# Optimization experiments

Measured on AMD Instinct MI355X. Metric: run time of the kernel, lower is better.

The kernel has to match this reference:

```python
import jax, jax.numpy as jnp
import numpy as np

CUTOFF = 2.0
LOG2 = float(np.log(2.0))

def ssp(x):
    # shifted softplus: softplus(x) - log(2)
    return jax.nn.softplus(x) - LOG2

def setup_inputs() -> dict:
    key = jax.random.key(0)
    ks = jax.random.split(key, 12)
    N, E, H, F, G = 10000, 320000, 256, 256, 50
    x = jax.random.normal(ks[0], (N, H), dtype=jnp.float32)
    edge_index = jax.random.randint(ks[1], (2, E), 0, N, dtype=jnp.int64)
    edge_weight = jax.random.normal(ks[2], (E, 3), dtype=jnp.float32)
    edge_attr = jax.random.normal(ks[3], (E, G), dtype=jnp.float32)
    s = lambda fan_in: 1.0 / np.sqrt(fan_in)
    mlp_w1 = jax.random.uniform(ks[4], (G, F), jnp.float32, -s(G), s(G))
    mlp_b1 = jax.random.uniform(ks[5], (F,), jnp.float32, -s(G), s(G))
    mlp_w2 = jax.random.uniform(ks[6], (F, F), jnp.float32, -s(F), s(F))
    mlp_b2 = jax.random.uniform(ks[7], (F,), jnp.float32, -s(F), s(F))
    lin1_w = jax.random.uniform(ks[8], (H, F), jnp.float32, -s(H), s(H))
    lin2_w = jax.random.uniform(ks[9], (F, H), jnp.float32, -s(F), s(F))
    lin2_b = jax.random.uniform(ks[10], (H,), jnp.float32, -s(F), s(F))
    return {"x": x, "edge_index": edge_index, "edge_weight": edge_weight,
            "edge_attr": edge_attr, "mlp_w1": mlp_w1, "mlp_b1": mlp_b1,
            "mlp_w2": mlp_w2, "mlp_b2": mlp_b2, "lin1_w": lin1_w,
            "lin2_w": lin2_w, "lin2_b": lin2_b}

def reference(x, edge_index, edge_weight, edge_attr,
              mlp_w1, mlp_b1, mlp_w2, mlp_b2, lin1_w, lin2_w, lin2_b):
    N = x.shape[0]
    # cutoff envelope on edge distances
    distances = jnp.linalg.norm(edge_weight, axis=1)                 # [E]
    C = 0.5 * (jnp.cos(distances * jnp.pi / CUTOFF) + 1.0)
    C = C * (distances <= CUTOFF)                                    # [E]
    # edge filter MLP
    W = ssp(edge_attr @ mlp_w1 + mlp_b1) @ mlp_w2 + mlp_b2           # [E, F]
    W = W * C[:, None]
    i, j = edge_index[0], edge_index[1]
    messages = W * (x[j] @ lin1_w)                                   # [E, F]
    agg = jax.ops.segment_sum(messages, i, num_segments=N)           # [N, F]
    h = ssp(agg @ lin2_w + lin2_b)                                   # [N, H]
    return x + h
```

## Files before the change

### kernel.cpp

```cpp
#include <hip/hip_runtime.h>
#include <hip/hip_bf16.h>
#include <stdint.h>

#define HF 256
#define GG 50

typedef __attribute__((ext_vector_type(8))) short bf16x8;
typedef __attribute__((ext_vector_type(4))) short bf16x4;
typedef __attribute__((ext_vector_type(4))) float f32x4;

__device__ __forceinline__ uint32_t f2bf2u(float a, float b){
    __hip_bfloat162 h = __float22bfloat162_rn(make_float2(a, b));
    union { __hip_bfloat162 h; uint32_t u; } v; v.h = h; return v.u;
}
__device__ __forceinline__ float bf2f(short s){
    union { uint32_t u; float f; } v; v.u = ((uint32_t)(uint16_t)s) << 16;
    return v.f;
}
__device__ __forceinline__ float ssp_f(float x){
    float e = __builtin_amdgcn_exp2f(x * 1.44269504088896341f);
    return 0.69314718055994531f * __builtin_amdgcn_logf(1.0f + e)
         - 0.69314718055994531f;
}

__device__ __forceinline__ void pack_natural(const float* __restrict__ B,
                                             short* __restrict__ Bp,
                                             int idx, int KT, int kmax)
{
    int lane = idx & 63;
    int kt   = (idx >> 6) & (KT - 1);
    int ntg  = idx >> (6 + (KT == 2 ? 1 : 3));
    int col  = ntg * 16 + (lane & 15);
    int k0   = kt * 32 + (lane >> 4) * 8;
    uint32_t u[4];
#pragma unroll
    for (int jj = 0; jj < 4; ++jj) {
        int ka = k0 + 2*jj, kb = ka + 1;
        float a = (ka < kmax) ? B[(size_t)ka * HF + col] : 0.f;
        float b = (kb < kmax) ? B[(size_t)kb * HF + col] : 0.f;
        u[jj] = f2bf2u(a, b);
    }
    *(uint4*)&Bp[(size_t)idx * 8] = *(uint4*)u;
}

__global__ __launch_bounds__(256)
void prep_kernel(const float* __restrict__ w1, const float* __restrict__ b1,
                 const float* __restrict__ w2,
                 const float* __restrict__ lin1, const float* __restrict__ lin2,
                 short* __restrict__ w1p, short* __restrict__ w2p,
                 short* __restrict__ lin1p, short* __restrict__ lin2p,
                 const float* __restrict__ x, short* __restrict__ x_bf, int nx8,
                 const int* __restrict__ eidx, int* __restrict__ cnt, int E,
                 float* __restrict__ agg, int nAgg4, int gConv, int gHist)
{
    int b = blockIdx.x, tid = threadIdx.x;
    if (b < 8) {
        int idx  = b * 256 + tid;
        int lane = idx & 63;
        int kt   = (idx >> 6) & 1;
        int ntg  = idx >> 7;
        int col  = ntg * 16 + (lane & 15);
        int k0   = kt * 32 + (lane >> 4) * 8;
        uint32_t u[4];
#pragma unroll
        for (int jj = 0; jj < 4; ++jj) {
            int ka = k0 + 2*jj, kb = ka + 1;
            float va = (ka < GG) ? w1[(size_t)ka * HF + col]
                                 : ((ka == GG) ? b1[col] : 0.f);
            float vb = (kb < GG) ? w1[(size_t)kb * HF + col]
                                 : ((kb == GG) ? b1[col] : 0.f);
            u[jj] = f2bf2u(va, vb);
        }
        *(uint4*)&w1p[(size_t)idx * 8] = *(uint4*)u;
    } else if (b < 40) {
        int idx = (b - 8) * 256 + tid;
        int lane = idx & 63;
        int kt   = (idx >> 6) & 7;
        int ntg  = idx >> 9;
        int col  = ntg * 16 + (lane & 15);
        int s0   = kt * 32 + (lane >> 4) * 8;
        uint32_t u[4];
#pragma unroll
        for (int jj = 0; jj < 4; ++jj) {
            int sa = s0 + 2*jj, sb = sa + 1;
            int fa = (sa >> 6) * 64 + (sa & 3) * 16 + ((sa & 63) >> 2);
            int fb = (sb >> 6) * 64 + (sb & 3) * 16 + ((sb & 63) >> 2);
            u[jj] = f2bf2u(w2[(size_t)fa * HF + col], w2[(size_t)fb * HF + col]);
        }
        *(uint4*)&w2p[(size_t)idx * 8] = *(uint4*)u;
    } else if (b < 72) {
        pack_natural(lin1, lin1p, (b - 40) * 256 + tid, 8, HF);
    } else if (b < 104) {
        pack_natural(lin2, lin2p, (b - 72) * 256 + tid, 8, HF);
    } else if (b < 104 + gConv) {
        int idx = (b - 104) * 256 + tid;
        if (idx < nx8) {
            const float* xp = x + (size_t)idx * 8;
            float4 p0 = *(const float4*)(xp);
            float4 p1 = *(const float4*)(xp + 4);
            uint32_t u[4] = { f2bf2u(p0.x, p0.y), f2bf2u(p0.z, p0.w),
                              f2bf2u(p1.x, p1.y), f2bf2u(p1.z, p1.w) };
            *(uint4*)&x_bf[(size_t)idx * 8] = *(uint4*)u;
        }
    } else if (b < 104 + gConv + gHist) {
        int e = (b - 104 - gConv) * 256 + tid;
        if (e < E) atomicAdd(&cnt[eidx[e]], 1);
    } else {
        int idx = (b - 104 - gConv - gHist) * 256 + tid;
        if (idx < nAgg4) ((float4*)agg)[idx] = make_float4(0.f, 0.f, 0.f, 0.f);
    }
}

__global__ __launch_bounds__(256)
void scan_kernel(const int* __restrict__ cnt, int* __restrict__ row,
                 int* __restrict__ cursor, int N, int E)
{
    __shared__ int part[256];
    const int t = threadIdx.x;
    const int CH = (N + 255) / 256;
    int lo = t * CH;
    int hi = min(lo + CH, N);
    int s = 0;
    for (int n = lo; n < hi; ++n) s += cnt[n];
    part[t] = s;
    __syncthreads();
    for (int off = 1; off < 256; off <<= 1) {
        int v = (t >= off) ? part[t - off] : 0;
        __syncthreads();
        part[t] += v;
        __syncthreads();
    }
    int acc = part[t] - s;
    for (int n = lo; n < hi; ++n) {
        row[n] = acc; cursor[n] = acc;
        acc += cnt[n];
    }
    if (t == 255) row[N] = E;
}

__global__ __launch_bounds__(256)
void mid_kernel(const int* __restrict__ eidx, int* __restrict__ cursor,
                int* __restrict__ perm, int E, int gScatter,
                const short* __restrict__ x_bf, const short* __restrict__ lin1p,
                short* __restrict__ y_p, int N)
{
    const int tid = threadIdx.x;
    if ((int)blockIdx.x < gScatter) {
        int e = blockIdx.x * 256 + tid;
        if (e < E) {
            int pos = atomicAdd(&cursor[eidx[e]], 1);
            perm[pos] = e;
        }
        return;
    }
    const int blk  = blockIdx.x - gScatter;
    const int lane = tid & 63;
    const int w    = tid >> 6;
    const int l15  = lane & 15;
    const int quad = lane >> 4;
    const int row0 = blk * 32;

    f32x4 acc[2][4];
#pragma unroll
    for (int mt = 0; mt < 2; ++mt)
#pragma unroll
        for (int nt = 0; nt < 4; ++nt) acc[mt][nt] = (f32x4){0.f,0.f,0.f,0.f};

#pragma unroll 2
    for (int kt = 0; kt < 8; ++kt) {
        bf16x8 af[2];
#pragma unroll
        for (int mt = 0; mt < 2; ++mt) {
            int r = row0 + mt * 16 + l15;
            int rl = (r < N) ? r : 0;
            af[mt] = *(const bf16x8*)&x_bf[(size_t)rl * HF + kt * 32 + quad * 8];
        }
#pragma unroll
        for (int nt = 0; nt < 4; ++nt) {
            bf16x8 bfr = *(const bf16x8*)&lin1p[(size_t)(((w*4+nt)*8+kt)*64+lane)*8];
#pragma unroll
            for (int mt = 0; mt < 2; ++mt)
                acc[mt][nt] = __builtin_amdgcn_mfma_f32_16x16x32_bf16(af[mt], bfr, acc[mt][nt], 0, 0, 0);
        }
    }
#pragma unroll
    for (int mt = 0; mt < 2; ++mt) {
#pragma unroll
        for (int r = 0; r < 4; ++r) {
            int row = row0 + mt * 16 + quad * 4 + r;
            if (row < N) {
                uint2 u = make_uint2(f2bf2u(acc[mt][0][r], acc[mt][1][r]),
                                     f2bf2u(acc[mt][2][r], acc[mt][3][r]));
                *(uint2*)&y_p[(size_t)row * HF + w * 64 + l15 * 4] = u;
            }
        }
    }
}

__global__ __launch_bounds__(256)
void node2_kernel(const float* __restrict__ agg, const short* __restrict__ lin2p,
                  const float* __restrict__ bias, const float* __restrict__ x,
                  float* __restrict__ out, int N)
{
    const int tid  = threadIdx.x;
    const int lane = tid & 63;
    const int w    = tid >> 6;
    const int l15  = lane & 15;
    const int quad = lane >> 4;
    const int row0 = blockIdx.x * 32;

    f32x4 acc[2][4];
#pragma unroll
    for (int mt = 0; mt < 2; ++mt)
#pragma unroll
        for (int nt = 0; nt < 4; ++nt) acc[mt][nt] = (f32x4){0.f,0.f,0.f,0.f};

#pragma unroll 2
    for (int kt = 0; kt < 8; ++kt) {
        bf16x8 af[2];
#pragma unroll
        for (int mt = 0; mt < 2; ++mt) {
            int r = row0 + mt * 16 + l15;
            int rl = (r < N) ? r : 0;
            const float* ap = agg + (size_t)rl * HF + kt * 32 + quad * 8;
            float4 p0 = *(const float4*)(ap);
            float4 p1 = *(const float4*)(ap + 4);
            union { uint32_t u[4]; bf16x8 v; } c;
            c.u[0] = f2bf2u(p0.x, p0.y); c.u[1] = f2bf2u(p0.z, p0.w);
            c.u[2] = f2bf2u(p1.x, p1.y); c.u[3] = f2bf2u(p1.z, p1.w);
            af[mt] = c.v;
        }
#pragma unroll
        for (int nt = 0; nt < 4; ++nt) {
            bf16x8 bfr = *(const bf16x8*)&lin2p[(size_t)(((w*4+nt)*8+kt)*64+lane)*8];
#pragma unroll
            for (int mt = 0; mt < 2; ++mt)
                acc[mt][nt] = __builtin_amdgcn_mfma_f32_16x16x32_bf16(af[mt], bfr, acc[mt][nt], 0, 0, 0);
        }
    }
    float bs[4];
#pragma unroll
    for (int nt = 0; nt < 4; ++nt) bs[nt] = bias[w * 64 + nt * 16 + l15];
#pragma unroll
    for (int mt = 0; mt < 2; ++mt) {
#pragma unroll
        for (int r = 0; r < 4; ++r) {
            int row = row0 + mt * 16 + quad * 4 + r;
            if (row < N) {
#pragma unroll
                for (int nt = 0; nt < 4; ++nt) {
                    int f = w * 64 + nt * 16 + l15;
                    float v = ssp_f(acc[mt][nt][r] + bs[nt]) + x[(size_t)row * HF + f];
                    out[(size_t)row * HF + f] = v;
                }
            }
        }
    }
}

__global__ __launch_bounds__(256, 4)
void edge_mfma(const float* __restrict__ ea, const int* __restrict__ eidx,
               const float* __restrict__ ew,
               const short* __restrict__ w1p,
               const short* __restrict__ w2p, const float* __restrict__ b2,
               const short* __restrict__ y_p, const int* __restrict__ perm,
               const int* __restrict__ rowp,
               float* __restrict__ agg, int E)
{
    __shared__ short smem[19456];
    short* ea_b = smem;
    short* hid  = smem;
    short* msgT = smem;
    short* St   = smem + 18432;
    __shared__ int s_e[64], s_i[64], s_j[64];
    __shared__ float s_c[64];
    __shared__ int s_runnode[64];
    __shared__ unsigned char s_runcomp[64];
    __shared__ unsigned long long s_bmask;
    __shared__ int s_runcnt;

    const int tid  = threadIdx.x;
    const int lane = tid & 63;
    const int w    = tid >> 6;
    const int l15  = lane & 15;
    const int quad = lane >> 4;
    const int e0   = blockIdx.x * 64;

    if (tid < 64) {
        int pp = e0 + tid;
        int e = 0, iv = -1, jv = 0;
        float c = 0.f;
        if (pp < E) {
            e  = perm[pp];
            iv = eidx[e];
            jv = eidx[E + e];
            float d0 = ew[e*3+0], d1 = ew[e*3+1], d2 = ew[e*3+2];
            float d = sqrtf(d0*d0 + d1*d1 + d2*d2);
            c = (d <= 2.0f) ? 0.5f * (__cosf(d * 1.57079632679489662f) + 1.0f) : 0.f;
        }
        s_e[tid] = e; s_i[tid] = iv; s_j[tid] = jv; s_c[tid] = c;
        int ivn = __shfl_down(iv, 1);
        bool flag = (tid == 63) || (iv != ivn);
        unsigned long long m = __ballot(flag);
        if (flag) {
            int rid = (int)__popcll(m & ((1ull << tid) - 1ull));
            s_runnode[rid] = iv;
            int comp = 0;
            if (iv >= 0) {
                int lo = rowp[iv], hi = rowp[iv + 1];
                comp = (lo >= e0 && hi <= e0 + 64) ? 1 : 0;
            }
            s_runcomp[rid] = (unsigned char)comp;
        }
        if (tid == 0) { s_bmask = m; s_runcnt = (int)__popcll(m); }
    }
    __syncthreads();

    for (int idx = tid; idx < 64 * 25; idx += 256) {
        int e = idx / 25, q = idx - e * 25;
        const float* sp = ea + (size_t)s_e[e] * GG + q * 2;
        float2 v = *(const float2*)sp;
        *(uint32_t*)&ea_b[e * 72 + q * 2] = f2bf2u(v.x, v.y);
    }
    for (int idx = tid; idx < 64 * 7; idx += 256) {
        int e = idx / 7, q = idx - e * 7;
        *(uint32_t*)&ea_b[e * 72 + 50 + q * 2] = (q == 0) ? 0x00003F80u : 0u;
    }
    __syncthreads();

    f32x4 acc1[4][4];
#pragma unroll
    for (int mt = 0; mt < 4; ++mt)
#pragma unroll
        for (int nt = 0; nt < 4; ++nt) acc1[mt][nt] = (f32x4){0.f,0.f,0.f,0.f};

#pragma unroll
    for (int kt = 0; kt < 2; ++kt) {
        bf16x8 af[4];
#pragma unroll
        for (int mt = 0; mt < 4; ++mt)
            af[mt] = *(bf16x8*)&ea_b[(mt * 16 + l15) * 72 + kt * 32 + quad * 8];
#pragma unroll
        for (int nt = 0; nt < 4; ++nt) {
            bf16x8 bfr = *(const bf16x8*)&w1p[(size_t)(((w*4+nt)*2+kt)*64+lane)*8];
#pragma unroll
            for (int mt = 0; mt < 4; ++mt)
                acc1[mt][nt] = __builtin_amdgcn_mfma_f32_16x16x32_bf16(af[mt], bfr, acc1[mt][nt], 0, 0, 0);
        }
    }
    __syncthreads();

#pragma unroll
    for (int mt = 0; mt < 4; ++mt) {
#pragma unroll
        for (int r = 0; r < 4; ++r) {
            int e = mt * 16 + quad * 4 + r;
            float v0 = ssp_f(acc1[mt][0][r]);
            float v1 = ssp_f(acc1[mt][1][r]);
            float v2 = ssp_f(acc1[mt][2][r]);
            float v3 = ssp_f(acc1[mt][3][r]);
            uint2 u = make_uint2(f2bf2u(v0, v1), f2bf2u(v2, v3));
            *(uint2*)&hid[e * 264 + w * 64 + l15 * 4] = u;
        }
    }
    __syncthreads();

    bf16x4 yv[4][4];
#pragma unroll
    for (int mt = 0; mt < 4; ++mt)
#pragma unroll
        for (int r = 0; r < 4; ++r) {
            int e = mt * 16 + quad * 4 + r;
            yv[mt][r] = *(const bf16x4*)&y_p[(size_t)s_j[e] * HF + w * 64 + l15 * 4];
        }

    f32x4 acc2[4][4];
#pragma unroll
    for (int mt = 0; mt < 4; ++mt)
#pragma unroll
        for (int nt = 0; nt < 4; ++nt) acc2[mt][nt] = (f32x4){0.f,0.f,0.f,0.f};

#pragma unroll 2
    for (int kt = 0; kt < 8; ++kt) {
        bf16x8 af[4];
#pragma unroll
        for (int mt = 0; mt < 4; ++mt)
            af[mt] = *(bf16x8*)&hid[(mt * 16 + l15) * 264 + kt * 32 + quad * 8];
#pragma unroll
        for (int nt = 0; nt < 4; ++nt) {
            bf16x8 bfr = *(const bf16x8*)&w2p[(size_t)(((w*4+nt)*8+kt)*64+lane)*8];
#pragma unroll
            for (int mt = 0; mt < 4; ++mt)
                acc2[mt][nt] = __builtin_amdgcn_mfma_f32_16x16x32_bf16(af[mt], bfr, acc2[mt][nt], 0, 0, 0);
        }
    }
    __syncthreads();

    float bias2[4];
#pragma unroll
    for (int nt = 0; nt < 4; ++nt) bias2[nt] = b2[w * 64 + nt * 16 + l15];
    float cs[4][4];
#pragma unroll
    for (int mt = 0; mt < 4; ++mt)
#pragma unroll
        for (int r = 0; r < 4; ++r)
            cs[mt][r] = s_c[mt * 16 + quad * 4 + r];
#pragma unroll
    for (int mt = 0; mt < 4; ++mt) {
#pragma unroll
        for (int nt = 0; nt < 4; ++nt) {
            int col = w * 64 + nt * 16 + l15;
            float v0 = (acc2[mt][nt][0] + bias2[nt]) * cs[mt][0] * bf2f(yv[mt][0][nt]);
            float v1 = (acc2[mt][nt][1] + bias2[nt]) * cs[mt][1] * bf2f(yv[mt][1][nt]);
            float v2 = (acc2[mt][nt][2] + bias2[nt]) * cs[mt][2] * bf2f(yv[mt][2][nt]);
            float v3 = (acc2[mt][nt][3] + bias2[nt]) * cs[mt][3] * bf2f(yv[mt][3][nt]);
            uint2 u = make_uint2(f2bf2u(v0, v1), f2bf2u(v2, v3));
            *(uint2*)&msgT[col * 72 + mt * 16 + quad * 4] = u;
        }
    }
    {
        unsigned long long bm = s_bmask;
        int e   = tid & 63;
        int rb  = tid >> 6;
        int rid = (int)__popcll(bm & ((1ull << e) - 1ull));
#pragma unroll
        for (int q = 0; q < 4; ++q) {
            int r = rb + q * 4;
            St[r * 64 + e] = (rid == r) ? (short)0x3F80 : (short)0;
        }
    }
    __syncthreads();

    const int runcnt = s_runcnt;
    for (int ntg = 0; ntg * 16 < runcnt; ++ntg) {
        if (ntg > 0) {
            __syncthreads();
            unsigned long long bm = s_bmask;
            int e   = tid & 63;
            int rb  = tid >> 6;
            int rid = (int)__popcll(bm & ((1ull << e) - 1ull));
#pragma unroll
            for (int q = 0; q < 4; ++q) {
                int r = rb + q * 4;
                St[r * 64 + e] = (rid == ntg * 16 + r) ? (short)0x3F80 : (short)0;
            }
            __syncthreads();
        }
        f32x4 acc3[4];
#pragma unroll
        for (int mt = 0; mt < 4; ++mt) acc3[mt] = (f32x4){0.f,0.f,0.f,0.f};
#pragma unroll
        for (int kt = 0; kt < 2; ++kt) {
            bf16x8 bS = *(bf16x8*)&St[l15 * 64 + kt * 32 + quad * 8];
#pragma unroll
            for (int mt = 0; mt < 4; ++mt) {
                bf16x8 af = *(bf16x8*)&msgT[(w*64 + mt*16 + l15) * 72 + kt*32 + quad*8];
                acc3[mt] = __builtin_amdgcn_mfma_f32_16x16x32_bf16(af, bS, acc3[mt], 0, 0, 0);
            }
        }
        int r = ntg * 16 + l15;
        if (r < runcnt) {
            int node = s_runnode[r];
            if (node >= 0) {
                float* ap = agg + (size_t)node * HF + w * 64 + quad * 4;
                if (s_runcomp[r]) {
#pragma unroll
                    for (int mt = 0; mt < 4; ++mt) {
                        float4 v = make_float4(acc3[mt][0], acc3[mt][1], acc3[mt][2], acc3[mt][3]);
                        *(float4*)(ap + mt * 16) = v;
                    }
                } else {
#pragma unroll
                    for (int mt = 0; mt < 4; ++mt)
#pragma unroll
                        for (int g = 0; g < 4; ++g)
                            atomicAdd(ap + mt * 16 + g, acc3[mt][g]);
                }
            }
        }
    }
}

extern "C" void kernel_launch(void* const* d_in, const int* in_sizes, int n_in,
                              void* d_out, int out_size, void* d_ws, size_t ws_size,
                              hipStream_t stream)
{
    const float* x     = (const float*)d_in[0];
    const int*   eidx  = (const int*)  d_in[1];
    const float* ew    = (const float*)d_in[2];
    const float* ea    = (const float*)d_in[3];
    const float* w1    = (const float*)d_in[4];
    const float* b1    = (const float*)d_in[5];
    const float* w2    = (const float*)d_in[6];
    const float* b2    = (const float*)d_in[7];
    const float* lin1  = (const float*)d_in[8];
    const float* lin2  = (const float*)d_in[9];
    const float* lin2b = (const float*)d_in[10];
    float* out = (float*)d_out;

    const int N = in_sizes[0] / HF;
    const int E = in_sizes[2] / 3;

    const size_t fN = (size_t)N * HF;
    float* agg    = (float*)d_ws;
    short* y_p    = (short*)(agg + fN);
    short* x_bf   = y_p + fN;
    int*   cnt    = (int*)(x_bf + fN);
    int*   row    = cnt + N;
    int*   cursor = row + (N + 8);
    int*   perm   = cursor + N;
    short* w1p    = (short*)(((uintptr_t)(perm + E) + 255) & ~(uintptr_t)255);
    short* w2p    = w1p + 16384;
    short* lin1p  = w2p + 65536;
    short* lin2p  = lin1p + 65536;

    hipMemsetAsync(cnt, 0, (size_t)N * sizeof(int), stream);

    const int nx8   = (int)(fN / 8);
    const int nAgg4 = (int)(fN / 4);
    const int gConv = (nx8 + 255) / 256;
    const int gHist = (E + 255) / 256;
    const int gZero = (nAgg4 + 255) / 256;
    prep_kernel<<<dim3(104 + gConv + gHist + gZero), dim3(256), 0, stream>>>(
        w1, b1, w2, lin1, lin2, w1p, w2p, lin1p, lin2p, x, x_bf, nx8,
        eidx, cnt, E, agg, nAgg4, gConv, gHist);

    scan_kernel<<<dim3(1), dim3(256), 0, stream>>>(cnt, row, cursor, N, E);

    const int gScatter = (E + 255) / 256;
    const int gNode    = (N + 31) / 32;
    mid_kernel<<<dim3(gScatter + gNode), dim3(256), 0, stream>>>(
        eidx, cursor, perm, E, gScatter, x_bf, lin1p, y_p, N);

    edge_mfma<<<dim3((E + 63) / 64), dim3(256), 0, stream>>>(
        ea, eidx, ew, w1p, w2p, b2, y_p, perm, row, agg, E);

    node2_kernel<<<dim3(gNode), dim3(256), 0, stream>>>(
        agg, lin2p, lin2b, x, out, N);
}
```

Baseline: 358.9 us.

## Load edge attributes directly into MFMA fragments and overlap scan with node GEMM

```diff
diff --git a/kernel.cpp b/kernel.cpp
--- a/kernel.cpp
+++ b/kernel.cpp
@@ -8,6 +8,7 @@
 typedef __attribute__((ext_vector_type(8))) short bf16x8;
 typedef __attribute__((ext_vector_type(4))) short bf16x4;
 typedef __attribute__((ext_vector_type(4))) float f32x4;
+typedef float f32x4a __attribute__((ext_vector_type(4), aligned(4)));
 
 __device__ __forceinline__ uint32_t f2bf2u(float a, float b){
     __hip_bfloat162 h = __float22bfloat162_rn(make_float2(a, b));
@@ -112,53 +113,40 @@
 }
 
 __global__ __launch_bounds__(256)
-void scan_kernel(const int* __restrict__ cnt, int* __restrict__ row,
-                 int* __restrict__ cursor, int N, int E)
-{
-    __shared__ int part[256];
-    const int t = threadIdx.x;
-    const int CH = (N + 255) / 256;
-    int lo = t * CH;
-    int hi = min(lo + CH, N);
-    int s = 0;
-    for (int n = lo; n < hi; ++n) s += cnt[n];
-    part[t] = s;
-    __syncthreads();
-    for (int off = 1; off < 256; off <<= 1) {
-        int v = (t >= off) ? part[t - off] : 0;
+void gemm_scan_kernel(const short* __restrict__ x_bf, const short* __restrict__ lin1p,
+                      short* __restrict__ y_p, int N,
+                      const int* __restrict__ cnt, int* __restrict__ row,
+                      int* __restrict__ cursor, int E, int gNode)
+{
+    const int tid = threadIdx.x;
+    if ((int)blockIdx.x >= gNode) {
+        __shared__ int part[256];
+        const int CH = (N + 255) / 256;
+        int lo = tid * CH;
+        int hi = min(lo + CH, N);
+        int s = 0;
+        for (int n = lo; n < hi; ++n) s += cnt[n];
+        part[tid] = s;
         __syncthreads();
-        part[t] += v;
-        __syncthreads();
-    }
-    int acc = part[t] - s;
-    for (int n = lo; n < hi; ++n) {
-        row[n] = acc; cursor[n] = acc;
-        acc += cnt[n];
-    }
-    if (t == 255) row[N] = E;
-}
-
-__global__ __launch_bounds__(256)
-void mid_kernel(const int* __restrict__ eidx, int* __restrict__ cursor,
-                int* __restrict__ perm, int E, int gScatter,
-                const short* __restrict__ x_bf, const short* __restrict__ lin1p,
-                short* __restrict__ y_p, int N)
-{
-    const int tid = threadIdx.x;
-    if ((int)blockIdx.x < gScatter) {
-        int e = blockIdx.x * 256 + tid;
-        if (e < E) {
-            int pos = atomicAdd(&cursor[eidx[e]], 1);
-            perm[pos] = e;
-        }
+        for (int off = 1; off < 256; off <<= 1) {
+            int v = (tid >= off) ? part[tid - off] : 0;
+            __syncthreads();
+            part[tid] += v;
+            __syncthreads();
+        }
+        int acc = part[tid] - s;
+        for (int n = lo; n < hi; ++n) {
+            row[n] = acc; cursor[n] = acc;
+            acc += cnt[n];
+        }
+        if (tid == 255) row[N] = E;
         return;
     }
-    const int blk  = blockIdx.x - gScatter;
     const int lane = tid & 63;
     const int w    = tid >> 6;
     const int l15  = lane & 15;
     const int quad = lane >> 4;
-    const int row0 = blk * 32;
+    const int row0 = blockIdx.x * 32;
 
     f32x4 acc[2][4];
 #pragma unroll
@@ -187,13 +175,24 @@
     for (int mt = 0; mt < 2; ++mt) {
 #pragma unroll
         for (int r = 0; r < 4; ++r) {
-            int row = row0 + mt * 16 + quad * 4 + r;
-            if (row < N) {
+            int row_ = row0 + mt * 16 + quad * 4 + r;
+            if (row_ < N) {
                 uint2 u = make_uint2(f2bf2u(acc[mt][0][r], acc[mt][1][r]),
                                      f2bf2u(acc[mt][2][r], acc[mt][3][r]));
-                *(uint2*)&y_p[(size_t)row * HF + w * 64 + l15 * 4] = u;
+                *(uint2*)&y_p[(size_t)row_ * HF + w * 64 + l15 * 4] = u;
             }
         }
+    }
+}
+
+__global__ __launch_bounds__(256)
+void scatter_kernel(const int* __restrict__ eidx, int* __restrict__ cursor,
+                    int* __restrict__ perm, int E)
+{
+    int e = blockIdx.x * 256 + threadIdx.x;
+    if (e < E) {
+        int pos = atomicAdd(&cursor[eidx[e]], 1);
+        perm[pos] = e;
     }
 }
 
@@ -245,13 +244,13 @@
     for (int mt = 0; mt < 2; ++mt) {
 #pragma unroll
         for (int r = 0; r < 4; ++r) {
-            int row = row0 + mt * 16 + quad * 4 + r;
-            if (row < N) {
+            int row_ = row0 + mt * 16 + quad * 4 + r;
+            if (row_ < N) {
 #pragma unroll
                 for (int nt = 0; nt < 4; ++nt) {
                     int f = w * 64 + nt * 16 + l15;
-                    float v = ssp_f(acc[mt][nt][r] + bs[nt]) + x[(size_t)row * HF + f];
-                    out[(size_t)row * HF + f] = v;
+                    float v = ssp_f(acc[mt][nt][r] + bs[nt]) + x[(size_t)row_ * HF + f];
+                    out[(size_t)row_ * HF + f] = v;
                 }
             }
         }
@@ -267,17 +266,12 @@
                const int* __restrict__ rowp,
                float* __restrict__ agg, int E)
 {
-    __shared__ short smem[19456];
-    short* ea_b = smem;
+    __shared__ short smem[19584];
     short* hid  = smem;
     short* msgT = smem;
     short* St   = smem + 18432;
-    __shared__ int s_e[64], s_i[64], s_j[64];
-    __shared__ float s_c[64];
     __shared__ int s_runnode[64];
     __shared__ unsigned char s_runcomp[64];
-    __shared__ unsigned long long s_bmask;
-    __shared__ int s_runcnt;
 
     const int tid  = threadIdx.x;
     const int lane = tid & 63;
@@ -286,69 +280,89 @@
     const int quad = lane >> 4;
     const int e0   = blockIdx.x * 64;
 
-    if (tid < 64) {
-        int pp = e0 + tid;
-        int e = 0, iv = -1, jv = 0;
-        float c = 0.f;
-        if (pp < E) {
-            e  = perm[pp];
-            iv = eidx[e];
-            jv = eidx[E + e];
-            float d0 = ew[e*3+0], d1 = ew[e*3+1], d2 = ew[e*3+2];
-            float d = sqrtf(d0*d0 + d1*d1 + d2*d2);
-            c = (d <= 2.0f) ? 0.5f * (__cosf(d * 1.57079632679489662f) + 1.0f) : 0.f;
-        }
-        s_e[tid] = e; s_i[tid] = iv; s_j[tid] = jv; s_c[tid] = c;
-        int ivn = __shfl_down(iv, 1);
-        bool flag = (tid == 63) || (iv != ivn);
-        unsigned long long m = __ballot(flag);
-        if (flag) {
-            int rid = (int)__popcll(m & ((1ull << tid) - 1ull));
-            s_runnode[rid] = iv;
-            int comp = 0;
-            if (iv >= 0) {
-                int lo = rowp[iv], hi = rowp[iv + 1];
-                comp = (lo >= e0 && hi <= e0 + 64) ? 1 : 0;
-            }
-            s_runcomp[rid] = (unsigned char)comp;
-        }
-        if (tid == 0) { s_bmask = m; s_runcnt = (int)__popcll(m); }
-    }
-    __syncthreads();
-
-    for (int idx = tid; idx < 64 * 25; idx += 256) {
-        int e = idx / 25, q = idx - e * 25;
-        const float* sp = ea + (size_t)s_e[e] * GG + q * 2;
-        float2 v = *(const float2*)sp;
-        *(uint32_t*)&ea_b[e * 72 + q * 2] = f2bf2u(v.x, v.y);
-    }
-    for (int idx = tid; idx < 64 * 7; idx += 256) {
-        int e = idx / 7, q = idx - e * 7;
-        *(uint32_t*)&ea_b[e * 72 + 50 + q * 2] = (q == 0) ? 0x00003F80u : 0u;
-    }
-    __syncthreads();
+    int pp = e0 + lane;
+    int eL = 0, iv = -1;
+    float c = 0.f;
+    if (pp < E) {
+        eL = perm[pp];
+        iv = eidx[eL];
+        float d0 = ew[eL*3+0], d1 = ew[eL*3+1], d2 = ew[eL*3+2];
+        float d = sqrtf(d0*d0 + d1*d1 + d2*d2);
+        c = (d <= 2.0f) ? 0.5f * (__cosf(d * 1.57079632679489662f) + 1.0f) : 0.f;
+    }
+    int jv = eidx[E + eL];
+    int ivn = __shfl_down(iv, 1);
+    bool flag = (lane == 63) || (iv != ivn);
+    unsigned long long bm = __ballot(flag);
+    const int runcnt = (int)__popcll(bm);
+    if (w == 0 && flag) {
+        int rid = (int)__popcll(bm & ((1ull << lane) - 1ull));
+        s_runnode[rid] = iv;
+        int comp = 0;
+        if (iv >= 0) {
+            int lo = rowp[iv], hi = rowp[iv + 1];
+            comp = (lo >= e0 && hi <= e0 + 64) ? 1 : 0;
+        }
+        s_runcomp[rid] = (unsigned char)comp;
+    }
+
+    int rp4[4];
+#pragma unroll
+    for (int mt = 0; mt < 4; ++mt) {
+        int er = e0 + mt * 16 + l15;
+        rp4[mt] = (er < E) ? perm[er] : 0;
+    }
+    bf16x8 a1[4][2];
+#pragma unroll
+    for (int mt = 0; mt < 4; ++mt) {
+        const float* er = ea + (size_t)rp4[mt] * GG;
+        f32x4a p0 = *(const f32x4a*)(er + quad * 8);
+        f32x4a p1 = *(const f32x4a*)(er + quad * 8 + 4);
+        union { uint32_t u[4]; bf16x8 v; } ca;
+        ca.u[0] = f2bf2u(p0[0], p0[1]); ca.u[1] = f2bf2u(p0[2], p0[3]);
+        ca.u[2] = f2bf2u(p1[0], p1[1]); ca.u[3] = f2bf2u(p1[2], p1[3]);
+        a1[mt][0] = ca.v;
+        union { uint32_t u[4]; bf16x8 v; } cb;
+        if (quad < 2) {
+            f32x4a q0 = *(const f32x4a*)(er + 32 + quad * 8);
+            f32x4a q1 = *(const f32x4a*)(er + 36 + quad * 8);
+            cb.u[0] = f2bf2u(q0[0], q0[1]); cb.u[1] = f2bf2u(q0[2], q0[3]);
+            cb.u[2] = f2bf2u(q1[0], q1[1]); cb.u[3] = f2bf2u(q1[2], q1[3]);
+        } else if (quad == 2) {
+            float2 q = *(const float2*)(er + 48);
+            cb.u[0] = f2bf2u(q.x, q.y);
+            cb.u[1] = 0x00003F80u;
+            cb.u[2] = 0u; cb.u[3] = 0u;
+        } else {
+            cb.u[0] = 0u; cb.u[1] = 0u; cb.u[2] = 0u; cb.u[3] = 0u;
+        }
+        a1[mt][1] = cb.v;
+    }
 
     f32x4 acc1[4][4];
 #pragma unroll
     for (int mt = 0; mt < 4; ++mt)
 #pragma unroll
         for (int nt = 0; nt < 4; ++nt) acc1[mt][nt] = (f32x4){0.f,0.f,0.f,0.f};
-
 #pragma unroll
     for (int kt = 0; kt < 2; ++kt) {
-        bf16x8 af[4];
-#pragma unroll
-        for (int mt = 0; mt < 4; ++mt)
-            af[mt] = *(bf16x8*)&ea_b[(mt * 16 + l15) * 72 + kt * 32 + quad * 8];
 #pragma unroll
         for (int nt = 0; nt < 4; ++nt) {
             bf16x8 bfr = *(const bf16x8*)&w1p[(size_t)(((w*4+nt)*2+kt)*64+lane)*8];
 #pragma unroll
             for (int mt = 0; mt < 4; ++mt)
-                acc1[mt][nt] = __builtin_amdgcn_mfma_f32_16x16x32_bf16(af[mt], bfr, acc1[mt][nt], 0, 0, 0);
-        }
-    }
-    __syncthreads();
+                acc1[mt][nt] = __builtin_amdgcn_mfma_f32_16x16x32_bf16(a1[mt][kt], bfr, acc1[mt][nt], 0, 0, 0);
+        }
+    }
+
+    bf16x4 yv[4][4];
+#pragma unroll
+    for (int mt = 0; mt < 4; ++mt)
+#pragma unroll
+        for (int r = 0; r < 4; ++r) {
+            int j = __shfl(jv, mt * 16 + quad * 4 + r);
+            yv[mt][r] = *(const bf16x4*)&y_p[(size_t)j * HF + w * 64 + l15 * 4];
+        }
 
 #pragma unroll
     for (int mt = 0; mt < 4; ++mt) {
@@ -365,15 +379,6 @@
     }
     __syncthreads();
 
-    bf16x4 yv[4][4];
-#pragma unroll
-    for (int mt = 0; mt < 4; ++mt)
-#pragma unroll
-        for (int r = 0; r < 4; ++r) {
-            int e = mt * 16 + quad * 4 + r;
-            yv[mt][r] = *(const bf16x4*)&y_p[(size_t)s_j[e] * HF + w * 64 + l15 * 4];
-        }
-
     f32x4 acc2[4][4];
 #pragma unroll
     for (int mt = 0; mt < 4; ++mt)
@@ -404,7 +409,7 @@
     for (int mt = 0; mt < 4; ++mt)
 #pragma unroll
         for (int r = 0; r < 4; ++r)
-            cs[mt][r] = s_c[mt * 16 + quad * 4 + r];
+            cs[mt][r] = __shfl(c, mt * 16 + quad * 4 + r);
 #pragma unroll
     for (int mt = 0; mt < 4; ++mt) {
 #pragma unroll
@@ -419,30 +424,27 @@
         }
     }
     {
-        unsigned long long bm = s_bmask;
         int e   = tid & 63;
         int rb  = tid >> 6;
         int rid = (int)__popcll(bm & ((1ull << e) - 1ull));
 #pragma unroll
         for (int q = 0; q < 4; ++q) {
             int r = rb + q * 4;
-            St[r * 64 + e] = (rid == r) ? (short)0x3F80 : (short)0;
+            St[r * 72 + e] = (rid == r) ? (short)0x3F80 : (short)0;
         }
     }
     __syncthreads();
 
-    const int runcnt = s_runcnt;
     for (int ntg = 0; ntg * 16 < runcnt; ++ntg) {
         if (ntg > 0) {
             __syncthreads();
-            unsigned long long bm = s_bmask;
             int e   = tid & 63;
             int rb  = tid >> 6;
             int rid = (int)__popcll(bm & ((1ull << e) - 1ull));
 #pragma unroll
             for (int q = 0; q < 4; ++q) {
                 int r = rb + q * 4;
-                St[r * 64 + e] = (rid == ntg * 16 + r) ? (short)0x3F80 : (short)0;
+                St[r * 72 + e] = (rid == ntg * 16 + r) ? (short)0x3F80 : (short)0;
             }
             __syncthreads();
         }
@@ -451,7 +453,7 @@
         for (int mt = 0; mt < 4; ++mt) acc3[mt] = (f32x4){0.f,0.f,0.f,0.f};
 #pragma unroll
         for (int kt = 0; kt < 2; ++kt) {
-            bf16x8 bS = *(bf16x8*)&St[l15 * 64 + kt * 32 + quad * 8];
+            bf16x8 bS = *(bf16x8*)&St[l15 * 72 + kt * 32 + quad * 8];
 #pragma unroll
             for (int mt = 0; mt < 4; ++mt) {
                 bf16x8 af = *(bf16x8*)&msgT[(w*64 + mt*16 + l15) * 72 + kt*32 + quad*8];
@@ -525,12 +527,12 @@
         w1, b1, w2, lin1, lin2, w1p, w2p, lin1p, lin2p, x, x_bf, nx8,
         eidx, cnt, E, agg, nAgg4, gConv, gHist);
 
-    scan_kernel<<<dim3(1), dim3(256), 0, stream>>>(cnt, row, cursor, N, E);
+    const int gNode = (N + 31) / 32;
+    gemm_scan_kernel<<<dim3(gNode + 1), dim3(256), 0, stream>>>(
+        x_bf, lin1p, y_p, N, cnt, row, cursor, E, gNode);
 
     const int gScatter = (E + 255) / 256;
-    const int gNode    = (N + 31) / 32;
-    mid_kernel<<<dim3(gScatter + gNode), dim3(256), 0, stream>>>(
-        eidx, cursor, perm, E, gScatter, x_bf, lin1p, y_p, N);
+    scatter_kernel<<<dim3(gScatter), dim3(256), 0, stream>>>(eidx, cursor, perm, E);
 
     edge_mfma<<<dim3((E + 63) / 64), dim3(256), 0, stream>>>(
         ea, eidx, ew, w1p, w2p, b2, y_p, perm, row, agg, E);
```

Measured after the change: 403.7 us. +12.5%, slower.
